# Optimization experiments

Hardware: AMD Instinct MI355X
Metric: run time of the kernel (lower is better)

Reference implementation:

```python
import jax, jax.numpy as jnp
import numpy as np

B, N, F_IN, D, TOPK, HID = 64, 512, 256, 128, 20, 512


def setup_inputs() -> dict:
    key = jax.random.key(0)
    ks = jax.random.split(key, 10)
    s = lambda fan: 1.0 / np.sqrt(fan)
    return {
        "data": jax.random.normal(ks[0], (B, F_IN, N), jnp.float32),
        "emb_weight": jax.random.normal(ks[1], (N, D), jnp.float32) * s(D),      # nn.Embedding, kaiming-ish
        "lin_w": jax.random.normal(ks[2], (D, F_IN), jnp.float32) * s(F_IN),     # GraphLayer.lin (no bias)
        "att_i": jax.random.normal(ks[3], (D,), jnp.float32) * 0.1,
        "att_j": jax.random.normal(ks[4], (D,), jnp.float32) * 0.1,
        "att_em_i": jax.random.normal(ks[5], (D,), jnp.float32) * 0.1,
        "att_em_j": jax.random.normal(ks[6], (D,), jnp.float32) * 0.1,
        "gnn_bias": jnp.zeros((D,), jnp.float32),
        "bn_gamma": jnp.ones((D,), jnp.float32),
        "bn_beta": jnp.zeros((D,), jnp.float32),
        "w1": jax.random.normal(ks[7], (HID, N), jnp.float32) * s(N),            # Linear(node_num, hidden, bias=False)
        "w2": jax.random.normal(ks[8], (HID, HID), jnp.float32) * s(HID),        # Linear(hidden, hidden)
        "b2": jnp.zeros((HID,), jnp.float32),
    }


def reference(data, emb_weight, lin_w, att_i, att_j, att_em_i, att_em_j,
              gnn_bias, bn_gamma, bn_beta, w1, w2, b2):
    data = jax.lax.stop_gradient(data)                       # x = data.clone().detach()
    b, f_in, n = data.shape
    d = emb_weight.shape[1]
    x = jnp.transpose(data, (0, 2, 1)).reshape(b * n, f_in)  # [B*N, F]

    # --- dynamic graph from detached embedding: cosine topk ---
    W = jax.lax.stop_gradient(emb_weight)
    nrm = jnp.linalg.norm(W, axis=-1)
    cos = (W @ W.T) / (nrm[:, None] * nrm[None, :])
    topk_idx = jax.lax.top_k(cos, TOPK)[1]                   # [N, topk] (learned_graph)
    src = topk_idx.reshape(-1)                               # gated_j (sources)
    dst = jnp.repeat(jnp.arange(n), TOPK)                    # gated_i (destinations)
    offs = (jnp.arange(b) * n)[:, None]
    bsrc = (src[None, :] + offs).reshape(-1)                 # [B*N*topk]
    bdst = (dst[None, :] + offs).reshape(-1)

    # --- GDN GraphLayer (heads=1, concat=False, aggr=add) ---
    xl = x @ lin_w.T                                         # [B*N, D]
    emb_all = jnp.tile(emb_weight, (b, 1))                   # [B*N, D]
    xi, xj = xl[bdst], xl[bsrc]
    ei, ej = emb_all[bdst], emb_all[bsrc]
    alpha = xi @ att_i + ei @ att_em_i + xj @ att_j + ej @ att_em_j   # [E]
    alpha = jax.nn.leaky_relu(alpha, 0.2)
    amax = jax.ops.segment_max(alpha, bdst, num_segments=b * n)
    ex = jnp.exp(alpha - amax[bdst])
    denom = jax.ops.segment_sum(ex, bdst, num_segments=b * n)
    a = ex / denom[bdst]                                     # segment softmax over dest
    agg = jax.ops.segment_sum(xj * a[:, None], bdst, num_segments=b * n) + gnn_bias

    # --- BatchNorm1d (eval: mean 0, var 1) + ReLU ---
    h = agg * (bn_gamma / jnp.sqrt(1.0 + 1e-5)) + bn_beta
    gcn = jax.nn.relu(h).reshape(b, n, d)

    # --- embedding gate + linear block over node dim ---
    out = gcn * emb_weight[None]                             # [B, N, D]
    out = jnp.transpose(out, (0, 2, 1))                      # [B, D, N]
    out = out @ w1.T                                         # [B, D, HID]
    out = out @ w2.T + b2
    out = jax.nn.sigmoid(out)
    return out, emb_weight, topk_idx
```

## Files before the change

### kernel.cpp

```cpp
#include <hip/hip_runtime.h>
#include <hip/hip_bf16.h>

constexpr int B = 64, N = 512, F_IN = 256, D = 128, TOPK = 20, HID = 512;

typedef __attribute__((ext_vector_type(8))) short short8_t;
typedef __attribute__((ext_vector_type(4))) float f32x4;

__device__ inline short f2bs(float f) {
    union { __hip_bfloat16 h; short s; } u; u.h = __float2bfloat16(f); return u.s;
}
__device__ inline float bs2f(short s) {
    return __uint_as_float(((unsigned)(unsigned short)s) << 16);
}

template<int ITERS>
__device__ inline void stage_bf16(short* ldst, const short* __restrict__ src,
                                  int stride, int k0, int t) {
    #pragma unroll
    for (int i = 0; i < ITERS; ++i) {
        int lin = t + i * 256, row = lin >> 2, seg = lin & 3;
        *(short8_t*)&ldst[row * 40 + seg * 8] =
            *(const short8_t*)&src[(size_t)row * stride + k0 + seg * 8];
    }
}
template<int ITERS>
__device__ inline void stage_f32(short* ldst, const float* __restrict__ src,
                                 int stride, int k0, int t) {
    #pragma unroll
    for (int i = 0; i < ITERS; ++i) {
        int lin = t + i * 256, row = lin >> 2, seg = lin & 3;
        const float* p = &src[(size_t)row * stride + k0 + seg * 8];
        float4 x = *(const float4*)p, y = *(const float4*)(p + 4);
        short8_t v = { f2bs(x.x), f2bs(x.y), f2bs(x.z), f2bs(x.w),
                       f2bs(y.x), f2bs(y.y), f2bs(y.z), f2bs(y.w) };
        *(short8_t*)&ldst[row * 40 + seg * 8] = v;
    }
}

template<int MS, int NS>
__device__ inline void mfma_tiles(const short* lds_a, const short* lds_b,
                                  f32x4 (&acc)[MS][NS], int wm, int wn, int lr, int quad) {
    short8_t af[MS], bf[NS];
    #pragma unroll
    for (int ms = 0; ms < MS; ++ms)
        af[ms] = *(const short8_t*)&lds_a[(wm + ms * 16 + lr) * 40 + quad * 8];
    #pragma unroll
    for (int ns = 0; ns < NS; ++ns)
        bf[ns] = *(const short8_t*)&lds_b[(wn + ns * 16 + lr) * 40 + quad * 8];
    #pragma unroll
    for (int ms = 0; ms < MS; ++ms)
        #pragma unroll
        for (int ns = 0; ns < NS; ++ns)
            acc[ms][ns] = __builtin_amdgcn_mfma_f32_16x16x32_bf16(af[ms], bf[ns], acc[ms][ns], 0, 0, 0);
}

__global__ void k_norm(const float* __restrict__ W, const float* __restrict__ aei,
                       const float* __restrict__ aej, float* __restrict__ inv_norm,
                       float* __restrict__ ei, float* __restrict__ ej,
                       float* __restrict__ out_emb) {
    int n = blockIdx.x, t = threadIdx.x;
    float w = W[n * D + t];
    out_emb[n * D + t] = w;
    float s0 = w * w, s1 = w * aei[t], s2 = w * aej[t];
    #pragma unroll
    for (int o = 32; o > 0; o >>= 1) {
        s0 += __shfl_down(s0, o); s1 += __shfl_down(s1, o); s2 += __shfl_down(s2, o);
    }
    __shared__ float r[6];
    if ((t & 63) == 0) { int q = t >> 6; r[q * 3] = s0; r[q * 3 + 1] = s1; r[q * 3 + 2] = s2; }
    __syncthreads();
    if (t == 0) {
        inv_norm[n] = 1.0f / sqrtf(r[0] + r[3]);
        ei[n] = r[1] + r[4];
        ej[n] = r[2] + r[5];
    }
}

__global__ __launch_bounds__(256) void k_cos(const float* __restrict__ W,
                                             const float* __restrict__ inv_norm,
                                             float* __restrict__ cosm) {
    __shared__ float la[32][33];
    __shared__ float lb[32][33];
    int j0 = blockIdx.x * 32, i0 = blockIdx.y * 32, t = threadIdx.x;
    int ix = (t & 15) * 2, jx = (t >> 4) * 2;
    float acc[2][2] = {};
    for (int k0 = 0; k0 < D; k0 += 32) {
        #pragma unroll
        for (int i = 0; i < 4; ++i) {
            int lin = t + i * 256, rl = lin & 31, kk = lin >> 5;
            la[kk][rl] = W[(size_t)(i0 + rl) * D + k0 + kk];
            lb[kk][rl] = W[(size_t)(j0 + rl) * D + k0 + kk];
        }
        __syncthreads();
        #pragma unroll
        for (int kk = 0; kk < 32; ++kk) {
            float a0 = la[kk][ix], a1 = la[kk][ix + 1];
            float b0 = lb[kk][jx], b1 = lb[kk][jx + 1];
            acc[0][0] += a0 * b0; acc[0][1] += a0 * b1;
            acc[1][0] += a1 * b0; acc[1][1] += a1 * b1;
        }
        __syncthreads();
    }
    #pragma unroll
    for (int ii = 0; ii < 2; ++ii) {
        float inv_i = inv_norm[i0 + ix + ii];
        float2 v;
        v.x = acc[ii][0] * inv_i * inv_norm[j0 + jx + 0];
        v.y = acc[ii][1] * inv_i * inv_norm[j0 + jx + 1];
        *(float2*)&cosm[(size_t)(i0 + ix + ii) * N + j0 + jx] = v;
    }
}

__global__ __launch_bounds__(256) void k_sel(const float* __restrict__ cosm,
                                             int* __restrict__ topk,
                                             float* __restrict__ out_idx) {
    int t = threadIdx.x, wid = t >> 6, lane = t & 63;
    int i = blockIdx.x * 4 + wid;
    float4 p0 = *(const float4*)&cosm[(size_t)i * N + lane * 8];
    float4 p1 = *(const float4*)&cosm[(size_t)i * N + lane * 8 + 4];
    float v[8] = {p0.x, p0.y, p0.z, p0.w, p1.x, p1.y, p1.z, p1.w};
    for (int k = 0; k < TOPK; ++k) {
        float bv = v[0]; int bc = 0;
        #pragma unroll
        for (int c = 1; c < 8; ++c) if (v[c] > bv) { bv = v[c]; bc = c; }
        int bj = lane * 8 + bc;
        #pragma unroll
        for (int o = 1; o < 64; o <<= 1) {
            float ov = __shfl_xor(bv, o);
            int  oj = __shfl_xor(bj, o);
            if (ov > bv || (ov == bv && oj < bj)) { bv = ov; bj = oj; }
        }
        if (lane == 0) {
            topk[i * TOPK + k] = bj;
            out_idx[i * TOPK + k] = (float)bj;
        }
        int oc = bj & 7; bool owner = (bj >> 3) == lane;
        #pragma unroll
        for (int c = 0; c < 8; ++c) if (owner && c == oc) v[c] = -INFINITY;
    }
}

__global__ __launch_bounds__(256) void k_xl(const float* __restrict__ data,
                                            const float* __restrict__ lin_w,
                                            const float* __restrict__ att_i,
                                            const float* __restrict__ att_j,
                                            const float* __restrict__ ei,
                                            const float* __restrict__ ej,
                                            short* __restrict__ xlb,
                                            float* __restrict__ s_i,
                                            float* __restrict__ s_j) {
    __shared__ float lt[32][65];
    __shared__ __align__(16) short lds_a[64 * 40];
    __shared__ __align__(16) short lds_b[128 * 40];
    __shared__ float sred[2][64][2];
    int n0 = blockIdx.x * 64, b = blockIdx.y, t = threadIdx.x;
    int wid = t >> 6, lane = t & 63;
    int wm = (wid & 1) * 32, wn = (wid >> 1) * 64;
    int lr = lane & 15, quad = lane >> 4;
    f32x4 acc[2][4] = {};
    for (int k0 = 0; k0 < F_IN; k0 += 32) {
        {
            int f = t >> 3, ng = (t & 7) * 8;
            const float* p = &data[((size_t)b * F_IN + k0 + f) * N + n0 + ng];
            float4 v0 = *(const float4*)p, v1 = *(const float4*)(p + 4);
            float* q = &lt[f][ng];
            q[0] = v0.x; q[1] = v0.y; q[2] = v0.z; q[3] = v0.w;
            q[4] = v1.x; q[5] = v1.y; q[6] = v1.z; q[7] = v1.w;
        }
        stage_f32<2>(lds_b, lin_w, F_IN, k0, t);
        __syncthreads();
        {
            int row = t >> 2, seg = t & 3;
            short8_t a;
            #pragma unroll
            for (int j = 0; j < 8; ++j) a[j] = f2bs(lt[seg * 8 + j][row]);
            *(short8_t*)&lds_a[row * 40 + seg * 8] = a;
        }
        __syncthreads();
        mfma_tiles<2, 4>(lds_a, lds_b, acc, wm, wn, lr, quad);
        __syncthreads();
    }
    #pragma unroll
    for (int ms = 0; ms < 2; ++ms)
        #pragma unroll
        for (int ns = 0; ns < 4; ++ns) {
            int mb = wm + ms * 16 + quad * 4, col = wn + ns * 16 + lr;
            #pragma unroll
            for (int r = 0; r < 4; ++r)
                xlb[((size_t)b * N + n0 + mb + r) * D + col] = f2bs(acc[ms][ns][r]);
        }
    float si8[8], sj8[8];
    #pragma unroll
    for (int ms = 0; ms < 2; ++ms)
        #pragma unroll
        for (int r = 0; r < 4; ++r) {
            float si = 0.f, sj = 0.f;
            #pragma unroll
            for (int ns = 0; ns < 4; ++ns) {
                int col = wn + ns * 16 + lr;
                float x = acc[ms][ns][r];
                si += x * att_i[col];
                sj += x * att_j[col];
            }
            si8[ms * 4 + r] = si; sj8[ms * 4 + r] = sj;
        }
    #pragma unroll
    for (int o = 1; o < 16; o <<= 1) {
        #pragma unroll
        for (int i = 0; i < 8; ++i) {
            si8[i] += __shfl_xor(si8[i], o);
            sj8[i] += __shfl_xor(sj8[i], o);
        }
    }
    if (lr == 0) {
        #pragma unroll
        for (int ms = 0; ms < 2; ++ms)
            #pragma unroll
            for (int r = 0; r < 4; ++r) {
                int row = wm + ms * 16 + quad * 4 + r;
                sred[wid >> 1][row][0] = si8[ms * 4 + r];
                sred[wid >> 1][row][1] = sj8[ms * 4 + r];
            }
    }
    __syncthreads();
    if (t < 64) {
        int n = n0 + t;
        s_i[b * N + n] = sred[0][t][0] + sred[1][t][0] + ei[n];
        s_j[b * N + n] = sred[0][t][1] + sred[1][t][1] + ej[n];
    }
}

__global__ __launch_bounds__(256) void k_attn2(const short* __restrict__ xlb,
                                               const float* __restrict__ emb,
                                               const int* __restrict__ topk,
                                               const float* __restrict__ s_i,
                                               const float* __restrict__ s_j,
                                               const float* __restrict__ gnn_bias,
                                               const float* __restrict__ bn_gamma,
                                               const float* __restrict__ bn_beta,
                                               short* __restrict__ Gt) {
    __shared__ float alph[16][20];
    __shared__ int   js[16][20];
    __shared__ float lt[16][129];
    int n0 = blockIdx.x * 16, b = blockIdx.y, t = threadIdx.x;
    for (int e = t; e < 16 * TOPK; e += 256) {
        int nl = e / TOPK, k = e - nl * TOPK;
        int j = topk[(n0 + nl) * TOPK + k];
        js[nl][k] = j;
        float al = s_i[b * N + n0 + nl] + s_j[b * N + j];
        alph[nl][k] = al >= 0.f ? al : 0.2f * al;
    }
    __syncthreads();
    if (t < 16) {
        float m = -INFINITY;
        for (int k = 0; k < TOPK; ++k) m = fmaxf(m, alph[t][k]);
        float s = 0.f;
        for (int k = 0; k < TOPK; ++k) { float e_ = expf(alph[t][k] - m); alph[t][k] = e_; s += e_; }
        float inv = 1.0f / s;
        for (int k = 0; k < TOPK; ++k) alph[t][k] *= inv;
    }
    __syncthreads();
    {
        int nl = t >> 4, dl = (t & 15) * 8;
        float a[8] = {};
        for (int k = 0; k < TOPK; ++k) {
            float w = alph[nl][k];
            short8_t xv = *(const short8_t*)&xlb[((size_t)b * N + js[nl][k]) * D + dl];
            #pragma unroll
            for (int c = 0; c < 8; ++c) a[c] += w * bs2f(xv[c]);
        }
        const float bnk = 0.9999950000374997f;
        #pragma unroll
        for (int c = 0; c < 8; ++c) {
            int d = dl + c;
            float h = (a[c] + gnn_bias[d]) * (bn_gamma[d] * bnk) + bn_beta[d];
            h = fmaxf(h, 0.f);
            lt[nl][d] = h * emb[(n0 + nl) * D + d];
        }
    }
    __syncthreads();
    {
        int d = t >> 1, half = t & 1;
        short8_t v;
        #pragma unroll
        for (int j = 0; j < 8; ++j) v[j] = f2bs(lt[half * 8 + j][d]);
        *(short8_t*)&Gt[((size_t)b * D + d) * N + n0 + half * 8] = v;
    }
}

__global__ __launch_bounds__(256) void k_gemm1(const short* __restrict__ Gt,
                                               const float* __restrict__ w1,
                                               short* __restrict__ out1) {
    __shared__ __align__(16) short lds_a[128 * 40];
    __shared__ __align__(16) short lds_b[64 * 40];
    int h0 = blockIdx.x * 64, b = blockIdx.y, t = threadIdx.x;
    int wid = t >> 6, lane = t & 63;
    int wm = (wid >> 1) * 64, wn = (wid & 1) * 32;
    int lr = lane & 15, quad = lane >> 4;
    f32x4 acc[4][2] = {};
    const short* Asrc = Gt + (size_t)b * D * N;
    const float* Bsrc = w1 + (size_t)h0 * N;
    for (int k0 = 0; k0 < N; k0 += 32) {
        stage_bf16<2>(lds_a, Asrc, N, k0, t);
        stage_f32<1>(lds_b, Bsrc, N, k0, t);
        __syncthreads();
        mfma_tiles<4, 2>(lds_a, lds_b, acc, wm, wn, lr, quad);
        __syncthreads();
    }
    #pragma unroll
    for (int ms = 0; ms < 4; ++ms)
        #pragma unroll
        for (int ns = 0; ns < 2; ++ns) {
            int mb = wm + ms * 16 + quad * 4, col = h0 + wn + ns * 16 + lr;
            #pragma unroll
            for (int r = 0; r < 4; ++r)
                out1[((size_t)b * D + mb + r) * HID + col] = f2bs(acc[ms][ns][r]);
        }
}

__global__ __launch_bounds__(256) void k_gemm2(const short* __restrict__ out1,
                                               const float* __restrict__ w2,
                                               const float* __restrict__ b2,
                                               float* __restrict__ out) {
    __shared__ __align__(16) short lds_a[128 * 40];
    __shared__ __align__(16) short lds_b[64 * 40];
    int h0 = blockIdx.x * 64, b = blockIdx.y, t = threadIdx.x;
    int wid = t >> 6, lane = t & 63;
    int wm = (wid >> 1) * 64, wn = (wid & 1) * 32;
    int lr = lane & 15, quad = lane >> 4;
    f32x4 acc[4][2] = {};
    const short* Asrc = out1 + (size_t)b * D * HID;
    const float* Bsrc = w2 + (size_t)h0 * HID;
    for (int k0 = 0; k0 < HID; k0 += 32) {
        stage_bf16<2>(lds_a, Asrc, HID, k0, t);
        stage_f32<1>(lds_b, Bsrc, HID, k0, t);
        __syncthreads();
        mfma_tiles<4, 2>(lds_a, lds_b, acc, wm, wn, lr, quad);
        __syncthreads();
    }
    #pragma unroll
    for (int ms = 0; ms < 4; ++ms)
        #pragma unroll
        for (int ns = 0; ns < 2; ++ns) {
            int mb = wm + ms * 16 + quad * 4, col = h0 + wn + ns * 16 + lr;
            float bias = b2[col];
            #pragma unroll
            for (int r = 0; r < 4; ++r)
                out[((size_t)b * D + mb + r) * HID + col] =
                    1.0f / (1.0f + expf(-(acc[ms][ns][r] + bias)));
        }
}

extern "C" void kernel_launch(void* const* d_in, const int* in_sizes, int n_in,
                              void* d_out, int out_size, void* d_ws, size_t ws_size,
                              hipStream_t stream) {
    const float* data     = (const float*)d_in[0];
    const float* emb      = (const float*)d_in[1];
    const float* lin_w    = (const float*)d_in[2];
    const float* att_i    = (const float*)d_in[3];
    const float* att_j    = (const float*)d_in[4];
    const float* att_em_i = (const float*)d_in[5];
    const float* att_em_j = (const float*)d_in[6];
    const float* gnn_bias = (const float*)d_in[7];
    const float* bn_gamma = (const float*)d_in[8];
    const float* bn_beta  = (const float*)d_in[9];
    const float* w1       = (const float*)d_in[10];
    const float* w2       = (const float*)d_in[11];
    const float* b2       = (const float*)d_in[12];
    float* out            = (float*)d_out;

    float* ws       = (float*)d_ws;
    float* inv_norm = ws;
    float* ei       = ws + 512;
    float* ej       = ws + 1024;
    int*   topk     = (int*)(ws + 1536);
    float* s_i      = ws + 1536 + N * TOPK;
    float* s_j      = s_i + B * N;
    short* S        = (short*)(ws + 77312);
    short* Gt       = S;
    short* out1     = S + (size_t)B * D * N;
    short* xlb      = S + 2 * (size_t)B * D * N;
    float* cosm     = (float*)S;

    float* out_emb = out + (size_t)B * D * HID;
    float* out_idx = out_emb + (size_t)N * D;

    hipLaunchKernelGGL(k_norm,  dim3(N),              dim3(D),   0, stream, emb, att_em_i, att_em_j, inv_norm, ei, ej, out_emb);
    hipLaunchKernelGGL(k_cos,   dim3(N / 32, N / 32), dim3(256), 0, stream, emb, inv_norm, cosm);
    hipLaunchKernelGGL(k_sel,   dim3(N / 4),          dim3(256), 0, stream, cosm, topk, out_idx);
    hipLaunchKernelGGL(k_xl,    dim3(N / 64, B),      dim3(256), 0, stream, data, lin_w, att_i, att_j, ei, ej, xlb, s_i, s_j);
    hipLaunchKernelGGL(k_attn2, dim3(N / 16, B),      dim3(256), 0, stream, xlb, emb, topk, s_i, s_j, gnn_bias, bn_gamma, bn_beta, Gt);
    hipLaunchKernelGGL(k_gemm1, dim3(HID / 64, B),    dim3(256), 0, stream, Gt, w1, out1);
    hipLaunchKernelGGL(k_gemm2, dim3(HID / 64, B),    dim3(256), 0, stream, out1, w2, b2, out);
}
```

Before: 189.8 us.

## Stage full weight panel in LDS once and load A fragments directly from global

```diff
diff --git a/kernel.cpp b/kernel.cpp
--- a/kernel.cpp
+++ b/kernel.cpp
@@ -13,45 +13,21 @@
     return __uint_as_float(((unsigned)(unsigned short)s) << 16);
 }
 
-template<int ITERS>
-__device__ inline void stage_bf16(short* ldst, const short* __restrict__ src,
-                                  int stride, int k0, int t) {
-    #pragma unroll
-    for (int i = 0; i < ITERS; ++i) {
-        int lin = t + i * 256, row = lin >> 2, seg = lin & 3;
-        *(short8_t*)&ldst[row * 40 + seg * 8] =
-            *(const short8_t*)&src[(size_t)row * stride + k0 + seg * 8];
-    }
-}
-template<int ITERS>
-__device__ inline void stage_f32(short* ldst, const float* __restrict__ src,
-                                 int stride, int k0, int t) {
-    #pragma unroll
-    for (int i = 0; i < ITERS; ++i) {
-        int lin = t + i * 256, row = lin >> 2, seg = lin & 3;
-        const float* p = &src[(size_t)row * stride + k0 + seg * 8];
-        float4 x = *(const float4*)p, y = *(const float4*)(p + 4);
+template<int NC, int K>
+__device__ inline void stageB(short* lds_b, const float* __restrict__ src, int t) {
+    constexpr int G = 256 / NC;
+    constexpr int GK = K / G;
+    int j = t & (NC - 1), g = t / NC;
+    const float* p = src + (size_t)j * K + g * GK;
+    #pragma unroll
+    for (int kk = 0; kk < GK; kk += 8) {
+        float4 x = *(const float4*)(p + kk);
+        float4 y = *(const float4*)(p + kk + 4);
         short8_t v = { f2bs(x.x), f2bs(x.y), f2bs(x.z), f2bs(x.w),
                        f2bs(y.x), f2bs(y.y), f2bs(y.z), f2bs(y.w) };
-        *(short8_t*)&ldst[row * 40 + seg * 8] = v;
-    }
-}
-
-template<int MS, int NS>
-__device__ inline void mfma_tiles(const short* lds_a, const short* lds_b,
-                                  f32x4 (&acc)[MS][NS], int wm, int wn, int lr, int quad) {
-    short8_t af[MS], bf[NS];
-    #pragma unroll
-    for (int ms = 0; ms < MS; ++ms)
-        af[ms] = *(const short8_t*)&lds_a[(wm + ms * 16 + lr) * 40 + quad * 8];
-    #pragma unroll
-    for (int ns = 0; ns < NS; ++ns)
-        bf[ns] = *(const short8_t*)&lds_b[(wn + ns * 16 + lr) * 40 + quad * 8];
-    #pragma unroll
-    for (int ms = 0; ms < MS; ++ms)
-        #pragma unroll
-        for (int ns = 0; ns < NS; ++ns)
-            acc[ms][ns] = __builtin_amdgcn_mfma_f32_16x16x32_bf16(af[ms], bf[ns], acc[ms][ns], 0, 0, 0);
+        int kg = g * GK + kk;
+        *(short8_t*)&lds_b[(kg >> 5) * (NC * 36) + j * 36 + (kg & 31)] = v;
+    }
 }
 
 __global__ void k_norm(const float* __restrict__ W, const float* __restrict__ aei,
@@ -149,84 +125,51 @@
                                             short* __restrict__ xlb,
                                             float* __restrict__ s_i,
                                             float* __restrict__ s_j) {
-    __shared__ float lt[32][65];
-    __shared__ __align__(16) short lds_a[64 * 40];
-    __shared__ __align__(16) short lds_b[128 * 40];
-    __shared__ float sred[2][64][2];
+    __shared__ __align__(16) short lds_b[8 * 128 * 36];
     int n0 = blockIdx.x * 64, b = blockIdx.y, t = threadIdx.x;
     int wid = t >> 6, lane = t & 63;
-    int wm = (wid & 1) * 32, wn = (wid >> 1) * 64;
-    int lr = lane & 15, quad = lane >> 4;
-    f32x4 acc[2][4] = {};
-    for (int k0 = 0; k0 < F_IN; k0 += 32) {
-        {
-            int f = t >> 3, ng = (t & 7) * 8;
-            const float* p = &data[((size_t)b * F_IN + k0 + f) * N + n0 + ng];
-            float4 v0 = *(const float4*)p, v1 = *(const float4*)(p + 4);
-            float* q = &lt[f][ng];
-            q[0] = v0.x; q[1] = v0.y; q[2] = v0.z; q[3] = v0.w;
-            q[4] = v1.x; q[5] = v1.y; q[6] = v1.z; q[7] = v1.w;
-        }
-        stage_f32<2>(lds_b, lin_w, F_IN, k0, t);
-        __syncthreads();
-        {
-            int row = t >> 2, seg = t & 3;
-            short8_t a;
-            #pragma unroll
-            for (int j = 0; j < 8; ++j) a[j] = f2bs(lt[seg * 8 + j][row]);
-            *(short8_t*)&lds_a[row * 40 + seg * 8] = a;
-        }
-        __syncthreads();
-        mfma_tiles<2, 4>(lds_a, lds_b, acc, wm, wn, lr, quad);
-        __syncthreads();
-    }
-    #pragma unroll
-    for (int ms = 0; ms < 2; ++ms)
-        #pragma unroll
-        for (int ns = 0; ns < 4; ++ns) {
-            int mb = wm + ms * 16 + quad * 4, col = wn + ns * 16 + lr;
-            #pragma unroll
-            for (int r = 0; r < 4; ++r)
-                xlb[((size_t)b * N + n0 + mb + r) * D + col] = f2bs(acc[ms][ns][r]);
-        }
-    float si8[8], sj8[8];
-    #pragma unroll
-    for (int ms = 0; ms < 2; ++ms)
-        #pragma unroll
-        for (int r = 0; r < 4; ++r) {
-            float si = 0.f, sj = 0.f;
-            #pragma unroll
-            for (int ns = 0; ns < 4; ++ns) {
-                int col = wn + ns * 16 + lr;
-                float x = acc[ms][ns][r];
-                si += x * att_i[col];
-                sj += x * att_j[col];
-            }
-            si8[ms * 4 + r] = si; sj8[ms * 4 + r] = sj;
-        }
-    #pragma unroll
-    for (int o = 1; o < 16; o <<= 1) {
-        #pragma unroll
-        for (int i = 0; i < 8; ++i) {
-            si8[i] += __shfl_xor(si8[i], o);
-            sj8[i] += __shfl_xor(sj8[i], o);
-        }
-    }
-    if (lr == 0) {
-        #pragma unroll
-        for (int ms = 0; ms < 2; ++ms)
-            #pragma unroll
-            for (int r = 0; r < 4; ++r) {
-                int row = wm + ms * 16 + quad * 4 + r;
-                sred[wid >> 1][row][0] = si8[ms * 4 + r];
-                sred[wid >> 1][row][1] = sj8[ms * 4 + r];
-            }
-    }
-    __syncthreads();
-    if (t < 64) {
-        int n = n0 + t;
-        s_i[b * N + n] = sred[0][t][0] + sred[1][t][0] + ei[n];
-        s_j[b * N + n] = sred[0][t][1] + sred[1][t][1] + ej[n];
+    int wm = wid * 16, lr = lane & 15, quad = lane >> 4;
+    stageB<128, 256>(lds_b, lin_w, t);
+    __syncthreads();
+    f32x4 acc[8] = {};
+    int arow = n0 + wm + lr;
+    #pragma unroll
+    for (int c = 0; c < 8; ++c) {
+        const float* ap = data + ((size_t)b * F_IN + c * 32 + quad * 8) * N + arow;
+        short8_t a;
+        #pragma unroll
+        for (int j = 0; j < 8; ++j) a[j] = f2bs(ap[(size_t)j * N]);
+        const short* bp = lds_b + c * (128 * 36) + lr * 36 + quad * 8;
+        #pragma unroll
+        for (int ns = 0; ns < 8; ++ns) {
+            short8_t bfr = *(const short8_t*)(bp + ns * 16 * 36);
+            acc[ns] = __builtin_amdgcn_mfma_f32_16x16x32_bf16(a, bfr, acc[ns], 0, 0, 0);
+        }
+    }
+    #pragma unroll
+    for (int ns = 0; ns < 8; ++ns) {
+        int col = ns * 16 + lr;
+        #pragma unroll
+        for (int r = 0; r < 4; ++r)
+            xlb[((size_t)b * N + n0 + wm + quad * 4 + r) * D + col] = f2bs(acc[ns][r]);
+    }
+    #pragma unroll
+    for (int r = 0; r < 4; ++r) {
+        float si = 0.f, sj = 0.f;
+        #pragma unroll
+        for (int ns = 0; ns < 8; ++ns) {
+            int col = ns * 16 + lr;
+            float x = acc[ns][r];
+            si += x * att_i[col];
+            sj += x * att_j[col];
+        }
+        #pragma unroll
+        for (int o = 1; o < 16; o <<= 1) { si += __shfl_xor(si, o); sj += __shfl_xor(sj, o); }
+        if (lr == 0) {
+            int n = n0 + wm + quad * 4 + r;
+            s_i[b * N + n] = si + ei[n];
+            s_j[b * N + n] = sj + ej[n];
+        }
     }
 }
 
@@ -291,27 +234,34 @@
 __global__ __launch_bounds__(256) void k_gemm1(const short* __restrict__ Gt,
                                                const float* __restrict__ w1,
                                                short* __restrict__ out1) {
-    __shared__ __align__(16) short lds_a[128 * 40];
-    __shared__ __align__(16) short lds_b[64 * 40];
+    __shared__ __align__(16) short lds_b[16 * 64 * 36];
     int h0 = blockIdx.x * 64, b = blockIdx.y, t = threadIdx.x;
     int wid = t >> 6, lane = t & 63;
-    int wm = (wid >> 1) * 64, wn = (wid & 1) * 32;
-    int lr = lane & 15, quad = lane >> 4;
-    f32x4 acc[4][2] = {};
-    const short* Asrc = Gt + (size_t)b * D * N;
-    const float* Bsrc = w1 + (size_t)h0 * N;
-    for (int k0 = 0; k0 < N; k0 += 32) {
-        stage_bf16<2>(lds_a, Asrc, N, k0, t);
-        stage_f32<1>(lds_b, Bsrc, N, k0, t);
-        __syncthreads();
-        mfma_tiles<4, 2>(lds_a, lds_b, acc, wm, wn, lr, quad);
-        __syncthreads();
-    }
-    #pragma unroll
-    for (int ms = 0; ms < 4; ++ms)
-        #pragma unroll
-        for (int ns = 0; ns < 2; ++ns) {
-            int mb = wm + ms * 16 + quad * 4, col = h0 + wn + ns * 16 + lr;
+    int wm = wid * 32, lr = lane & 15, quad = lane >> 4;
+    stageB<64, 512>(lds_b, w1 + (size_t)h0 * N, t);
+    __syncthreads();
+    f32x4 acc[2][4] = {};
+    const short* A = Gt + (size_t)b * D * N;
+    #pragma unroll
+    for (int c = 0; c < 16; ++c) {
+        short8_t a[2];
+        #pragma unroll
+        for (int ms = 0; ms < 2; ++ms)
+            a[ms] = *(const short8_t*)&A[(size_t)(wm + ms * 16 + lr) * N + c * 32 + quad * 8];
+        const short* bp = lds_b + c * (64 * 36) + lr * 36 + quad * 8;
+        #pragma unroll
+        for (int ns = 0; ns < 4; ++ns) {
+            short8_t bfr = *(const short8_t*)(bp + ns * 16 * 36);
+            #pragma unroll
+            for (int ms = 0; ms < 2; ++ms)
+                acc[ms][ns] = __builtin_amdgcn_mfma_f32_16x16x32_bf16(a[ms], bfr, acc[ms][ns], 0, 0, 0);
+        }
+    }
+    #pragma unroll
+    for (int ms = 0; ms < 2; ++ms)
+        #pragma unroll
+        for (int ns = 0; ns < 4; ++ns) {
+            int mb = wm + ms * 16 + quad * 4, col = h0 + ns * 16 + lr;
             #pragma unroll
             for (int r = 0; r < 4; ++r)
                 out1[((size_t)b * D + mb + r) * HID + col] = f2bs(acc[ms][ns][r]);
@@ -322,27 +272,34 @@
                                                const float* __restrict__ w2,
                                                const float* __restrict__ b2,
                                                float* __restrict__ out) {
-    __shared__ __align__(16) short lds_a[128 * 40];
-    __shared__ __align__(16) short lds_b[64 * 40];
+    __shared__ __align__(16) short lds_b[16 * 64 * 36];
     int h0 = blockIdx.x * 64, b = blockIdx.y, t = threadIdx.x;
     int wid = t >> 6, lane = t & 63;
-    int wm = (wid >> 1) * 64, wn = (wid & 1) * 32;
-    int lr = lane & 15, quad = lane >> 4;
-    f32x4 acc[4][2] = {};
-    const short* Asrc = out1 + (size_t)b * D * HID;
-    const float* Bsrc = w2 + (size_t)h0 * HID;
-    for (int k0 = 0; k0 < HID; k0 += 32) {
-        stage_bf16<2>(lds_a, Asrc, HID, k0, t);
-        stage_f32<1>(lds_b, Bsrc, HID, k0, t);
-        __syncthreads();
-        mfma_tiles<4, 2>(lds_a, lds_b, acc, wm, wn, lr, quad);
-        __syncthreads();
-    }
-    #pragma unroll
-    for (int ms = 0; ms < 4; ++ms)
-        #pragma unroll
-        for (int ns = 0; ns < 2; ++ns) {
-            int mb = wm + ms * 16 + quad * 4, col = h0 + wn + ns * 16 + lr;
+    int wm = wid * 32, lr = lane & 15, quad = lane >> 4;
+    stageB<64, 512>(lds_b, w2 + (size_t)h0 * HID, t);
+    __syncthreads();
+    f32x4 acc[2][4] = {};
+    const short* A = out1 + (size_t)b * D * HID;
+    #pragma unroll
+    for (int c = 0; c < 16; ++c) {
+        short8_t a[2];
+        #pragma unroll
+        for (int ms = 0; ms < 2; ++ms)
+            a[ms] = *(const short8_t*)&A[(size_t)(wm + ms * 16 + lr) * HID + c * 32 + quad * 8];
+        const short* bp = lds_b + c * (64 * 36) + lr * 36 + quad * 8;
+        #pragma unroll
+        for (int ns = 0; ns < 4; ++ns) {
+            short8_t bfr = *(const short8_t*)(bp + ns * 16 * 36);
+            #pragma unroll
+            for (int ms = 0; ms < 2; ++ms)
+                acc[ms][ns] = __builtin_amdgcn_mfma_f32_16x16x32_bf16(a[ms], bfr, acc[ms][ns], 0, 0, 0);
+        }
+    }
+    #pragma unroll
+    for (int ms = 0; ms < 2; ++ms)
+        #pragma unroll
+        for (int ns = 0; ns < 4; ++ns) {
+            int mb = wm + ms * 16 + quad * 4, col = h0 + ns * 16 + lr;
             float bias = b2[col];
             #pragma unroll
             for (int r = 0; r < 4; ++r)
```

Measured after the change: 213.6 us. +12.6%, slower.
